# Performance work log

Hardware: AMD Instinct MI355X
Metric: run time of the kernel (lower is better)

Reference implementation:

```python
import jax, jax.numpy as jnp
import numpy as np

D = 1024
E = 8
K = 2
NUM_ITER = 2
DT = 0.1
H = 64           # controller_hidden
CTX = 2 * D


def _gelu(t):
    return jax.nn.gelu(t, approximate=False)


def _inl(ctrl, x, v, mu):
    # ctrl: [T, 3D] -> alpha, beta, gate chunks of size D
    alpha_raw, beta_raw, gate_raw = jnp.split(ctrl, 3, axis=-1)
    alpha = jax.nn.sigmoid(alpha_raw)
    beta = jax.nn.softplus(beta_raw)
    gate = jax.nn.sigmoid(gate_raw)
    error = x - mu
    v_next = alpha * v - beta * error
    x_next = x + DT * gate * v_next
    return x_next, v_next


def setup_inputs() -> dict:
    key = jax.random.key(0)
    ks = jax.random.split(key, 20)
    s = 0.02
    inp = {
        'x': jax.random.normal(ks[0], (4, 4096, D), jnp.float32),
        # router MLP
        'w_r1': jax.random.normal(ks[1], (D, D // 4), jnp.float32) * s,
        'b_r1': jnp.zeros((D // 4,), jnp.float32),
        'w_r2': jax.random.normal(ks[2], (D // 4, E), jnp.float32) * s,
        'b_r2': jnp.zeros((E,), jnp.float32),
        # halt gate MLP
        'w_h1': jax.random.normal(ks[3], (D, D // 4), jnp.float32) * s,
        'b_h1': jnp.zeros((D // 4,), jnp.float32),
        'w_h2': jax.random.normal(ks[4], (D // 4, 1), jnp.float32) * s,
        'b_h2': jnp.zeros((1,), jnp.float32),
        # expert tables
        'expert_w1': jax.random.normal(ks[5], (E, CTX, H), jnp.float32) * s,
        'expert_b1': jnp.zeros((E, H), jnp.float32),
        'expert_w2': jax.random.normal(ks[6], (E, H, 3 * D), jnp.float32) * s,
        'expert_b2': jnp.zeros((E, 3 * D), jnp.float32),
        # shared expert
        'w_s1': jax.random.normal(ks[7], (CTX, H), jnp.float32) * s,
        'b_s1': jnp.zeros((H,), jnp.float32),
        'w_s2': jax.random.normal(ks[8], (H, 3 * D), jnp.float32) * s,
        'b_s2': jnp.zeros((3 * D,), jnp.float32),
        'shared_weight': jnp.asarray(0.5, jnp.float32),
        # refine MLP
        'w_f1': jax.random.normal(ks[9], (D, 2 * D), jnp.float32) * s,
        'b_f1': jnp.zeros((2 * D,), jnp.float32),
        'w_f2': jax.random.normal(ks[10], (2 * D, D), jnp.float32) * s,
        'b_f2': jnp.zeros((D,), jnp.float32),
        'integration_weight': jnp.full((D,), 0.5, jnp.float32),
        'mu': jnp.zeros((D,), jnp.float32),
    }
    return inp


def reference(x, w_r1, b_r1, w_r2, b_r2, w_h1, b_h1, w_h2, b_h2,
              expert_w1, expert_b1, expert_w2, expert_b2,
              w_s1, b_s1, w_s2, b_s2, shared_weight,
              w_f1, b_f1, w_f2, b_f2, integration_weight, mu):
    B, N, Dm = x.shape
    xf = x.reshape(B * N, Dm)                       # [T, D]

    # router: top-k over softmax probs, renormalized
    logits = _gelu(xf @ w_r1 + b_r1) @ w_r2 + b_r2  # [T, E]
    probs = jax.nn.softmax(logits, axis=-1)
    top_p, top_i = jax.lax.top_k(probs, K)          # [T, K]
    top_p = top_p / jnp.sum(top_p, axis=-1, keepdims=True)

    flat_idx = top_i.reshape(-1)                    # [T*K]
    flat_w = top_p.reshape(-1, 1)                   # [T*K, 1]

    v = jnp.zeros_like(xf)
    integrated = xf
    for _ in range(NUM_ITER):
        ctx = jnp.concatenate([integrated, v], axis=-1)     # [T, 2D]

        # shared expert path
        shared_ctrl = _gelu(ctx @ w_s1 + b_s1) @ w_s2 + b_s2
        x_shared, v_shared = _inl(shared_ctrl, integrated, v, mu)
        sw = jax.nn.sigmoid(shared_weight)

        # routed experts: gather per-token weights, per-token matvec
        ctx_e = jnp.repeat(ctx, K, axis=0)                  # [T*K, 2D]
        x_e = jnp.repeat(integrated, K, axis=0)
        v_e = jnp.repeat(v, K, axis=0)
        w1 = expert_w1[flat_idx]                            # [T*K, 2D, H]
        b1 = expert_b1[flat_idx]
        w2 = expert_w2[flat_idx]                            # [T*K, H, 3D]
        b2 = expert_b2[flat_idx]
        hidden = _gelu(jnp.einsum('tc,tch->th', ctx_e, w1) + b1)
        ctrl = jnp.einsum('th,tho->to', hidden, w2) + b2    # [T*K, 3D]
        x_r, v_r = _inl(ctrl, x_e, v_e, mu)
        x_r = (x_r * flat_w).reshape(B * N, K, Dm).sum(axis=1)
        v_r = (v_r * flat_w).reshape(B * N, K, Dm).sum(axis=1)

        x_next = sw * x_shared + (1.0 - sw) * x_r
        v_next = sw * v_shared + (1.0 - sw) * v_r

        halt = jax.nn.sigmoid(_gelu(x_next @ w_h1 + b_h1) @ w_h2 + b_h2)  # [T,1]
        refined = _gelu(x_next @ w_f1 + b_f1) @ w_f2 + b_f2               # [T,D]
        integrated = integrated + halt * refined * integration_weight
        v = v_next

    return integrated.reshape(B, N, Dm)
```

## Files before the change

kernel.cpp:

```cpp
#include <hip/hip_runtime.h>


#define TOK   16384
#define DDIM  1024
#define NEXP  8
#define DTC   0.1f
#define NDESC 320
#define GPAD  20480

using f32x4 = __attribute__((ext_vector_type(4))) float;
using bfv8  = __attribute__((ext_vector_type(8))) short;

__device__ __forceinline__ unsigned short f2bf(float x){
  unsigned u = __builtin_bit_cast(unsigned, x);
  u += 0x7fffu + ((u >> 16) & 1u);
  return (unsigned short)(u >> 16);
}
__device__ __forceinline__ float bf2f(unsigned short h){
  return __builtin_bit_cast(float, ((unsigned)h) << 16);
}
__device__ __forceinline__ float sigmf(float x){ return 1.0f/(1.0f+__expf(-x)); }
__device__ __forceinline__ float geluf(float x){
  float u = 1.595769122f * __builtin_fmaf(0.044715f*x*x, x, x);
  return x * sigmf(u);
}
__device__ __forceinline__ float softpf(float x){
  return fmaxf(x, 0.0f) + __logf(1.0f + __expf(-fabsf(x)));
}
__device__ __forceinline__ f32x4 mfma16(bfv8 a, bfv8 b, f32x4 c){
  return __builtin_amdgcn_mfma_f32_16x16x32_bf16(a, b, c, 0, 0, 0);
}
typedef __attribute__((address_space(1))) const void gvoid_t;
typedef __attribute__((address_space(3))) void svoid_t;
__device__ __forceinline__ void gload16(const void* g, void* l){
  __builtin_amdgcn_global_load_lds((gvoid_t*)g, (svoid_t*)l, 16, 0, 0);
}

__global__ __launch_bounds__(256) void transpose_cast(
    const float* __restrict__ src, unsigned short* __restrict__ dst, int R, int C)
{
  __shared__ float tile[32][33];
  size_t bo = (size_t)blockIdx.z * R * C;
  const float* s = src + bo;
  unsigned short* d = dst + bo;
  int c0 = blockIdx.x * 32, r0 = blockIdx.y * 32;
  int tx = threadIdx.x, ty = threadIdx.y;
  #pragma unroll
  for (int j = 0; j < 4; j++)
    tile[ty + 8*j][tx] = s[(size_t)(r0 + ty + 8*j) * C + c0 + tx];
  __syncthreads();
  #pragma unroll
  for (int j = 0; j < 4; j++)
    d[(size_t)(c0 + ty + 8*j) * R + r0 + tx] = f2bf(tile[tx][ty + 8*j]);
}

__global__ __launch_bounds__(256) void xinit_k(
    const float* __restrict__ xf, unsigned short* __restrict__ xb)
{
  const int n = TOK * 256;
  for (int i = blockIdx.x * 256 + threadIdx.x; i < n; i += gridDim.x * 256) {
    float4 f = ((const float4*)xf)[i];
    ushort4 u = {f2bf(f.x), f2bf(f.y), f2bf(f.z), f2bf(f.w)};
    ((ushort4*)xb)[i] = u;
  }
}

__global__ __launch_bounds__(256) void ctxb_k(
    const float* __restrict__ xf, const int* __restrict__ tokmap,
    unsigned short* __restrict__ ctx)
{
  const int g = blockIdx.x, tid = threadIdx.x;
  const int t = tokmap[g];
  if (tid < 128) {
    uint4 o4 = {0,0,0,0};
    if (t >= 0) {
      const float4* s = (const float4*)(xf + (size_t)t * 1024) + tid * 2;
      float4 f0 = s[0], f1 = s[1];
      unsigned short tmp[8] = {f2bf(f0.x), f2bf(f0.y), f2bf(f0.z), f2bf(f0.w),
                               f2bf(f1.x), f2bf(f1.y), f2bf(f1.z), f2bf(f1.w)};
      o4 = *(uint4*)tmp;
    }
    *(uint4*)&ctx[(size_t)g * 2048 + tid * 8] = o4;
  } else {
    *(uint4*)&ctx[(size_t)g * 2048 + 1024 + (tid - 128) * 8] = uint4{0,0,0,0};
  }
}

template<int EPI>
__global__ __launch_bounds__(256) void gemm_k(
    const unsigned short* __restrict__ A, int lda,
    const unsigned short* __restrict__ BT,
    const float* __restrict__ bias, const float* __restrict__ bias2,
    int Kd, int N,
    unsigned short* __restrict__ obf, unsigned short* __restrict__ obf2,
    const float* __restrict__ halt, const float* __restrict__ iw,
    float* __restrict__ integ, unsigned short* __restrict__ ctxX,
    const int* __restrict__ pf)
{
  __shared__ unsigned short As[128][64];
  __shared__ unsigned short Bs[128][64];
  const int total = gridDim.x * gridDim.y;
  const int bid = blockIdx.y * gridDim.x + blockIdx.x;
  const int swz = (bid & 7) * (total >> 3) + (bid >> 3);
  const int bx = swz % gridDim.x, by = swz / gridDim.x;

  const int tid  = threadIdx.x, lane = tid & 63, w = tid >> 6;
  const int wm   = w >> 1, wn = w & 1;
  const int gm0  = by * 128, gn0 = bx * 128;
  const int r8   = lane >> 3;
  const int sseg = (lane & 7) ^ r8;

  const unsigned short* aga[4];
  const unsigned short* bga[4];
  #pragma unroll
  for (int c = 0; c < 4; c++) {
    aga[c] = A  + (size_t)(gm0 + w*32 + c*8 + r8) * lda + sseg*8;
    bga[c] = BT + (size_t)(gn0 + w*32 + c*8 + r8) * Kd  + sseg*8;
  }

  f32x4 acc[4][4];
  #pragma unroll
  for (int i = 0; i < 4; i++)
    #pragma unroll
    for (int j = 0; j < 4; j++)
      acc[i][j] = f32x4{0.f,0.f,0.f,0.f};

  const int xr = (lane & 7) << 3;
  for (int k0 = 0; k0 < Kd; k0 += 64) {
    #pragma unroll
    for (int c = 0; c < 4; c++) gload16(aga[c] + k0, &As[w*32 + c*8][0]);
    #pragma unroll
    for (int c = 0; c < 4; c++) gload16(bga[c] + k0, &Bs[w*32 + c*8][0]);
    __syncthreads();
    #pragma unroll
    for (int kk = 0; kk < 64; kk += 32) {
      const int kof = kk + ((lane >> 4) << 3);
      bfv8 a[4], b[4];
      #pragma unroll
      for (int mf = 0; mf < 4; mf++)
        a[mf] = *(const bfv8*)&As[wm*64 + mf*16 + (lane & 15)][kof ^ xr];
      #pragma unroll
      for (int nf = 0; nf < 4; nf++)
        b[nf] = *(const bfv8*)&Bs[wn*64 + nf*16 + (lane & 15)][kof ^ xr];
      #pragma unroll
      for (int mf = 0; mf < 4; mf++)
        #pragma unroll
        for (int nf = 0; nf < 4; nf++)
          acc[mf][nf] = mfma16(a[mf], b[nf], acc[mf][nf]);
    }
    __syncthreads();
  }

  #pragma unroll
  for (int mf = 0; mf < 4; mf++) {
    #pragma unroll
    for (int nf = 0; nf < 4; nf++) {
      int col = gn0 + wn*64 + nf*16 + (lane & 15);
      float bc;
      if (EPI == 2) bc = (col < 2048) ? bias[col] : bias2[col - 2048];
      else          bc = bias[col];
      #pragma unroll
      for (int r = 0; r < 4; r++) {
        int row = gm0 + wm*64 + mf*16 + ((lane >> 4) << 2) + r;
        float v = acc[mf][nf][r] + bc;
        if (EPI == 0) {
          obf[(size_t)row * N + col] = f2bf(geluf(v));
        } else if (EPI == 2) {
          if (col < 2048) obf [(size_t)row * 2048 + col]         = f2bf(geluf(v));
          else            obf2[(size_t)row * 256 + (col - 2048)] = f2bf(geluf(v));
        } else {
          size_t ix = (size_t)row * DDIM + col;
          float nv = integ[ix] + halt[row] * v * iw[col];
          integ[ix] = nv;
          if (ctxX) ctxX[(size_t)pf[row] * 2048 + col] = f2bf(nv);
        }
      }
    }
  }
}

__global__ __launch_bounds__(256) void router_k(
    const unsigned short* __restrict__ h1, const float* __restrict__ w_r2,
    const float* __restrict__ b_r2, int* __restrict__ topi, float* __restrict__ topw)
{
  int t = blockIdx.x * 4 + (threadIdx.x >> 6);
  int lane = threadIdx.x & 63;
  const unsigned short* hp = h1 + (size_t)t * 256 + lane * 4;
  float hv[4];
  #pragma unroll
  for (int j = 0; j < 4; j++) hv[j] = bf2f(hp[j]);
  float acc[8];
  #pragma unroll
  for (int e = 0; e < 8; e++) acc[e] = 0.f;
  #pragma unroll
  for (int j = 0; j < 4; j++) {
    const float* wr = w_r2 + (size_t)(lane*4 + j) * 8;
    #pragma unroll
    for (int e = 0; e < 8; e++) acc[e] += hv[j] * wr[e];
  }
  #pragma unroll
  for (int off = 32; off > 0; off >>= 1)
    #pragma unroll
    for (int e = 0; e < 8; e++) acc[e] += __shfl_xor(acc[e], off);
  if (lane == 0) {
    float lg[8];
    #pragma unroll
    for (int e = 0; e < 8; e++) lg[e] = acc[e] + b_r2[e];
    int i0 = 0; float m0 = lg[0];
    #pragma unroll
    for (int e = 1; e < 8; e++) if (lg[e] > m0) { m0 = lg[e]; i0 = e; }
    int i1 = -1; float m1 = -3.4e38f;
    #pragma unroll
    for (int e = 0; e < 8; e++) if (e != i0 && lg[e] > m1) { m1 = lg[e]; i1 = e; }
    float w0 = 1.0f / (1.0f + expf(m1 - m0));
    topi[t*2] = i0; topi[t*2+1] = i1;
    topw[t*2] = w0; topw[t*2+1] = 1.0f - w0;
  }
}

__global__ __launch_bounds__(256) void haltgate_k(
    const unsigned short* __restrict__ h1, const float* __restrict__ w_h2,
    const float* __restrict__ b_h2, float* __restrict__ halt)
{
  int t = blockIdx.x * 4 + (threadIdx.x >> 6);
  int lane = threadIdx.x & 63;
  const unsigned short* hp = h1 + (size_t)t * 256 + lane * 4;
  float s = 0.f;
  #pragma unroll
  for (int j = 0; j < 4; j++) s += bf2f(hp[j]) * w_h2[lane*4 + j];
  #pragma unroll
  for (int off = 32; off > 0; off >>= 1) s += __shfl_xor(s, off);
  if (lane == 0) halt[t] = sigmf(s + b_h2[0]);
}

__global__ __launch_bounds__(256) void pairb_k(
    const int* __restrict__ topi, const float* __restrict__ topw,
    int* __restrict__ cnt, int* __restrict__ plist, float* __restrict__ wA)
{
  int t = blockIdx.x * 256 + threadIdx.x;
  int a = topi[2*t], b = topi[2*t+1];
  float wa = topw[2*t];
  if (a > b) { int tmp = a; a = b; b = tmp; wa = 1.0f - wa; }
  int pid = a * 8 + b;
  int pos = atomicAdd(&cnt[pid], 1);
  plist[pid * TOK + pos] = t;
  wA[t] = wa;
}

__global__ void desc_k(const int* __restrict__ cnt, int4* __restrict__ desc,
                       int* __restrict__ ndesc, int* __restrict__ pbase)
{
  if (threadIdx.x == 0 && blockIdx.x == 0) {
    int nt = 0, rb = 0;
    for (int p = 0; p < 64; p++) {
      pbase[p] = rb;
      int c = cnt[p];
      for (int o = 0; o < c; o += 64) {
        int rem = c - o; if (rem > 64) rem = 64;
        desc[nt] = make_int4(p, rb + o, rem, 0);
        nt++;
      }
      rb += (c + 63) & ~63;
    }
    ndesc[0] = nt;
  }
}

__global__ __launch_bounds__(256) void pmap_k(
    const int* __restrict__ cnt, const int* __restrict__ pbase,
    const int* __restrict__ plist, int* __restrict__ tokmap, int* __restrict__ pf)
{
  int pid = blockIdx.x;
  int pos = blockIdx.y * 256 + threadIdx.x;
  if (pos < cnt[pid]) {
    int t = plist[pid * TOK + pos];
    int g = pbase[pid] + pos;
    tokmap[g] = t;
    pf[t] = g;
  }
}

__global__ __launch_bounds__(256) void exp1t_k(
    const unsigned short* __restrict__ ctx,
    const int4* __restrict__ desc, const int* __restrict__ ndesc,
    const unsigned short* __restrict__ ew1T, const float* __restrict__ eb1,
    const unsigned short* __restrict__ ws1T, const float* __restrict__ bs1,
    unsigned short* __restrict__ hiddenG)
{
  __shared__ unsigned short As[64][64];
  __shared__ unsigned short Bs[192][64];
  const int dx = blockIdx.x;
  if (dx >= ndesc[0]) return;
  int4 dd = desc[dx];
  const int pid = dd.x, rbt = dd.y;
  const int e0 = pid >> 3, e1 = pid & 7;
  const unsigned short* w1b[3] = { ew1T + (size_t)e0 * 64 * 2048,
                                   ew1T + (size_t)e1 * 64 * 2048, ws1T };
  const float* b1b[3] = { eb1 + e0 * 64, eb1 + e1 * 64, bs1 };
  const int tid = threadIdx.x, lane = tid & 63, w = tid >> 6;

  const int arow = w*8 + (lane >> 3);
  const int sseg = (lane & 7) ^ (lane >> 3);
  const unsigned short* asrc[2];
  #pragma unroll
  for (int q = 0; q < 2; q++)
    asrc[q] = ctx + (size_t)(rbt + q*32 + arow) * 2048 + sseg * 8;
  const unsigned short* bsrc[3][2];
  #pragma unroll
  for (int p = 0; p < 3; p++)
    #pragma unroll
    for (int q = 0; q < 2; q++)
      bsrc[p][q] = w1b[p] + (size_t)(q*32 + arow) * 2048 + sseg * 8;

  f32x4 acc[3][4];
  #pragma unroll
  for (int p = 0; p < 3; p++)
    #pragma unroll
    for (int j = 0; j < 4; j++)
      acc[p][j] = f32x4{0.f,0.f,0.f,0.f};

  const int xr = (lane & 7) << 3;
  for (int k0 = 0; k0 < 2048; k0 += 64) {
    #pragma unroll
    for (int q = 0; q < 2; q++) gload16(asrc[q] + k0, &As[q*32 + w*8][0]);
    #pragma unroll
    for (int p = 0; p < 3; p++)
      #pragma unroll
      for (int q = 0; q < 2; q++)
        gload16(bsrc[p][q] + k0, &Bs[p*64 + q*32 + w*8][0]);
    __syncthreads();
    #pragma unroll
    for (int kk = 0; kk < 64; kk += 32) {
      const int kof = kk + ((lane >> 4) << 3);
      bfv8 a = *(const bfv8*)&As[w*16 + (lane & 15)][kof ^ xr];
      #pragma unroll
      for (int p = 0; p < 3; p++)
        #pragma unroll
        for (int nf = 0; nf < 4; nf++) {
          bfv8 b = *(const bfv8*)&Bs[p*64 + nf*16 + (lane & 15)][kof ^ xr];
          acc[p][nf] = mfma16(a, b, acc[p][nf]);
        }
    }
    __syncthreads();
  }

  #pragma unroll
  for (int p = 0; p < 3; p++) {
    #pragma unroll
    for (int nf = 0; nf < 4; nf++) {
      int col = nf*16 + (lane & 15);
      float bb = b1b[p][col];
      #pragma unroll
      for (int r = 0; r < 4; r++) {
        int row = w*16 + ((lane >> 4) << 2) + r;
        hiddenG[(size_t)(3*rbt + p*64 + row) * 64 + col] =
            f2bf(geluf(acc[p][nf][r] + bb));
      }
    }
  }
}

__global__ __launch_bounds__(256) void exp2r_k(
    const unsigned short* __restrict__ hiddenG,
    const int4* __restrict__ desc, const int* __restrict__ ndesc,
    const int* __restrict__ tokmap, const float* __restrict__ wA,
    const unsigned short* __restrict__ ew2T, const float* __restrict__ eb2,
    const unsigned short* __restrict__ ws2T, const float* __restrict__ bs2,
    const float* __restrict__ swp, const float* __restrict__ mu,
    unsigned short* __restrict__ ctx, unsigned short* __restrict__ xaccB)
{
  __shared__ unsigned short W2s[3][192][64];
  __shared__ int   s_tok[64];
  __shared__ float s_w[64];
  const int zq = blockIdx.x, dx = blockIdx.y;
  if (dx >= ndesc[0]) return;
  int4 dd = desc[dx];
  const int pid = dd.x, rbt = dd.y, cnt = dd.z;
  const int e0 = pid >> 3, e1 = pid & 7;
  const int tid = threadIdx.x, lane = tid & 63, w = tid >> 6;
  const float sw = sigmf(swp[0]);

  if (tid < 64) {
    int t = tokmap[rbt + tid]; if (t < 0) t = 0;
    s_tok[tid] = t; s_w[tid] = wA[t];
  }

  const unsigned short* w2b[3] = { ew2T + (size_t)e0*3072*64,
                                   ew2T + (size_t)e1*3072*64, ws2T };
  const float* b2b[3] = { eb2 + e0*3072, eb2 + e1*3072, bs2 };
  const int d0q  = zq * 256;
  const int srow = w*8 + (lane >> 3);
  const int sseg = (lane & 7) ^ (lane >> 3);
  const int xr   = (lane & 7) << 3;
  const int cr4  = (lane >> 4) << 2;
  const int arow = w*16 + (lane & 15);
  const int kof8 = (lane >> 4) << 3;

  bfv8 afr[3][2];
  #pragma unroll
  for (int p = 0; p < 3; p++)
    #pragma unroll
    for (int kk = 0; kk < 2; kk++)
      afr[p][kk] = *(const bfv8*)&hiddenG[
          (size_t)(3*rbt + p*64 + arow) * 64 + kk*32 + kof8];

  auto STAGE = [&](int b, int dcq, int path) {
    const int d00 = d0q + dcq*64;
    const unsigned short* w2 = w2b[path];
    #pragma unroll
    for (int q = 0; q < 6; q++) {
      int row  = q*32 + srow;
      int grow = (row >> 6)*1024 + d00 + (row & 63);
      gload16(w2 + (size_t)grow*64 + sseg*8, &W2s[b][q*32 + w*8][0]);
    }
  };

  STAGE(0, 0, 0);
  STAGE(1, 0, 1);
  int toks[4]; float wa4[4];
  float xx[4][4], vv[4][4];

  #pragma unroll
  for (int dcq = 0; dcq < 4; dcq++) {
    const int d00 = d0q + dcq*64;
    f32x4 A4[4], B4[4], C4[4], D4[4];
    #pragma unroll
    for (int cf = 0; cf < 4; cf++) {
      A4[cf] = f32x4{0.f,0.f,0.f,0.f}; B4[cf] = f32x4{0.f,0.f,0.f,0.f};
      C4[cf] = f32x4{0.f,0.f,0.f,0.f}; D4[cf] = f32x4{0.f,0.f,0.f,0.f};
    }
    #pragma unroll
    for (int path = 0; path < 3; path++) {
      const int ph = dcq*3 + path;
      if (ph == 0) {
        __syncthreads();
      } else if (ph == 11) {
        asm volatile("s_waitcnt vmcnt(0)" ::: "memory");
        __builtin_amdgcn_s_barrier();
        __builtin_amdgcn_sched_barrier(0);
      } else {
        asm volatile("s_waitcnt vmcnt(6)" ::: "memory");
        __builtin_amdgcn_s_barrier();
        __builtin_amdgcn_sched_barrier(0);
      }
      if (ph == 0) {
        #pragma unroll
        for (int r = 0; r < 4; r++) {
          int row = w*16 + cr4 + r;
          toks[r] = s_tok[row]; wa4[r] = s_w[row];
        }
        #pragma unroll
        for (int cf = 0; cf < 4; cf++) {
          int d = d00 + cf*16 + (lane & 15);
          #pragma unroll
          for (int r = 0; r < 4; r++) {
            size_t g = (size_t)(rbt + w*16 + cr4 + r);
            xx[cf][r] = bf2f(ctx[g*2048 + d]);
            vv[cf][r] = bf2f(ctx[g*2048 + 1024 + d]);
          }
        }
      }
      if (ph < 10) {
        const int phn = ph + 2;
        STAGE(phn % 3, phn / 3, phn % 3);
      }
      f32x4 acc[12];
      #pragma unroll
      for (int j = 0; j < 12; j++) acc[j] = f32x4{0.f,0.f,0.f,0.f};
      #pragma unroll
      for (int kk = 0; kk < 2; kk++) {
        const int kof = kk*32 + kof8;
        #pragma unroll
        for (int nf = 0; nf < 12; nf++) {
          bfv8 b = *(const bfv8*)&W2s[ph % 3][nf*16 + (lane & 15)][kof ^ xr];
          acc[nf] = mfma16(afr[path][kk], b, acc[nf]);
        }
      }
      const float* b2 = b2b[path];
      #pragma unroll
      for (int cf = 0; cf < 4; cf++) {
        int d = d00 + cf*16 + (lane & 15);
        float ba = b2[d], bb = b2[1024 + d], bg = b2[2048 + d];
        #pragma unroll
        for (int r = 0; r < 4; r++) {
          float cw = (path == 0) ? (1.f - sw) * wa4[r]
                   : (path == 1) ? (1.f - sw) * (1.f - wa4[r]) : sw;
          float al = sigmf(acc[cf][r] + ba);
          float be = softpf(acc[4 + cf][r] + bb);
          float ga = sigmf(acc[8 + cf][r] + bg);
          A4[cf][r] += cw * al;       B4[cf][r] += cw * be;
          C4[cf][r] += cw * ga * al;  D4[cf][r] += cw * ga * be;
        }
      }
    }
    #pragma unroll
    for (int cf = 0; cf < 4; cf++) {
      int d = d00 + cf*16 + (lane & 15);
      float muv = mu[d];
      #pragma unroll
      for (int r = 0; r < 4; r++) {
        int row = w*16 + cr4 + r;
        size_t g = (size_t)(rbt + row);
        float err = xx[cf][r] - muv;
        float vt = vv[cf][r] * A4[cf][r] - err * B4[cf][r];
        float gv = vv[cf][r] * C4[cf][r] - err * D4[cf][r];
        if (row < cnt) {
          xaccB[(size_t)toks[r]*1024 + d] = f2bf(xx[cf][r] + DTC * gv);
          ctx[g*2048 + 1024 + d]          = f2bf(vt);
        }
      }
    }
    if (dcq < 3) {
      const int dn = d00 + 64;
      #pragma unroll
      for (int cf = 0; cf < 4; cf++) {
        int d = dn + cf*16 + (lane & 15);
        #pragma unroll
        for (int r = 0; r < 4; r++) {
          size_t g = (size_t)(rbt + w*16 + cr4 + r);
          xx[cf][r] = bf2f(ctx[g*2048 + d]);
          vv[cf][r] = bf2f(ctx[g*2048 + 1024 + d]);
        }
      }
    }
  }
}

extern "C" void kernel_launch(void* const* d_in, const int* in_sizes, int n_in,
                              void* d_out, int out_size, void* d_ws, size_t ws_size,
                              hipStream_t stream)
{
  const float* x    = (const float*)d_in[0];
  const float* w_r1 = (const float*)d_in[1];
  const float* b_r1 = (const float*)d_in[2];
  const float* w_r2 = (const float*)d_in[3];
  const float* b_r2 = (const float*)d_in[4];
  const float* w_h1 = (const float*)d_in[5];
  const float* b_h1 = (const float*)d_in[6];
  const float* w_h2 = (const float*)d_in[7];
  const float* b_h2 = (const float*)d_in[8];
  const float* ew1  = (const float*)d_in[9];
  const float* eb1  = (const float*)d_in[10];
  const float* ew2  = (const float*)d_in[11];
  const float* eb2  = (const float*)d_in[12];
  const float* w_s1 = (const float*)d_in[13];
  const float* b_s1 = (const float*)d_in[14];
  const float* w_s2 = (const float*)d_in[15];
  const float* b_s2 = (const float*)d_in[16];
  const float* swt  = (const float*)d_in[17];
  const float* w_f1 = (const float*)d_in[18];
  const float* b_f1 = (const float*)d_in[19];
  const float* w_f2 = (const float*)d_in[20];
  const float* b_f2 = (const float*)d_in[21];
  const float* iw   = (const float*)d_in[22];
  const float* mu   = (const float*)d_in[23];
  float* out = (float*)d_out;

  char* ws = (char*)d_ws;
  size_t off = 0;
  auto take = [&](size_t bytes) -> char* {
    char* p = ws + off;
    off = (off + bytes + 255) & ~(size_t)255;
    return p;
  };
  const size_t TD4 = (size_t)TOK * DDIM * 4;
  unsigned short* xaccB = (unsigned short*)take((size_t)TOK * 1024 * 2);
  unsigned short* ctx   = (unsigned short*)take((size_t)GPAD * 2048 * 2);
  unsigned short* rh    = (unsigned short*)take((size_t)TOK * 2048 * 2);
  unsigned short* hiddenG = (unsigned short*)take((size_t)3 * GPAD * 64 * 2);
  unsigned short* h1 = (unsigned short*)take((size_t)TOK * 256 * 2);
  float* halt = (float*)take((size_t)TOK * 4);
  int*   topi = (int*)take((size_t)TOK * 2 * 4);
  float* topw = (float*)take((size_t)TOK * 2 * 4);
  int*   cnt  = (int*)take(64 * 4);
  int*   ndsc = (int*)take(64);
  int*   pbase= (int*)take(64 * 4);
  int4*  desc = (int4*)take((size_t)NDESC * 16);
  int*   plist= (int*)take((size_t)64 * TOK * 4);
  float* wAa  = (float*)take((size_t)TOK * 4);
  int*   tokmap = (int*)take((size_t)GPAD * 4);
  int*   pf     = (int*)take((size_t)TOK * 4);
  unsigned short* w_r1T = (unsigned short*)take((size_t)256 * 1024 * 2);
  unsigned short* wFH   = (unsigned short*)take((size_t)2304 * 1024 * 2);
  unsigned short* w_f2T = (unsigned short*)take((size_t)1024 * 2048 * 2);
  unsigned short* w_s1T = (unsigned short*)take((size_t)64 * 2048 * 2);
  unsigned short* w_s2T = (unsigned short*)take((size_t)3072 * 64 * 2);
  unsigned short* ew1T  = (unsigned short*)take((size_t)NEXP * 64 * 2048 * 2);
  unsigned short* ew2T  = (unsigned short*)take((size_t)NEXP * 3072 * 64 * 2);
  if (off > ws_size) return;

  hipMemcpyAsync(out, x, TD4, hipMemcpyDeviceToDevice, stream);
  hipMemsetAsync(cnt, 0, 64 * 4, stream);
  hipMemsetAsync(tokmap, 0xFF, (size_t)GPAD * 4, stream);

  dim3 tb(32, 8);
  transpose_cast<<<dim3(  8, 32, 1), tb, 0, stream>>>(w_r1, w_r1T, 1024,  256);
  transpose_cast<<<dim3( 64, 32, 1), tb, 0, stream>>>(w_f1, wFH, 1024, 2048);
  transpose_cast<<<dim3(  8, 32, 1), tb, 0, stream>>>(w_h1, wFH + (size_t)2048*1024, 1024, 256);
  transpose_cast<<<dim3( 32, 64, 1), tb, 0, stream>>>(w_f2, w_f2T, 2048, 1024);
  transpose_cast<<<dim3(  2, 64, 1), tb, 0, stream>>>(w_s1, w_s1T, 2048,   64);
  transpose_cast<<<dim3( 96,  2, 1), tb, 0, stream>>>(w_s2, w_s2T,   64, 3072);
  transpose_cast<<<dim3(  2, 64, 8), tb, 0, stream>>>(ew1,  ew1T,  2048,   64);
  transpose_cast<<<dim3( 96,  2, 8), tb, 0, stream>>>(ew2,  ew2T,    64, 3072);

  xinit_k<<<2048, 256, 0, stream>>>(x, xaccB);
  gemm_k<0><<<dim3(2, 128), 256, 0, stream>>>(
      xaccB, 1024, w_r1T, b_r1, nullptr, 1024, 256, h1, nullptr,
      nullptr, nullptr, nullptr, nullptr, nullptr);
  router_k<<<TOK / 4, 256, 0, stream>>>(h1, w_r2, b_r2, topi, topw);
  pairb_k<<<TOK / 256, 256, 0, stream>>>(topi, topw, cnt, plist, wAa);
  desc_k<<<1, 64, 0, stream>>>(cnt, desc, ndsc, pbase);
  pmap_k<<<dim3(64, 64), 256, 0, stream>>>(cnt, pbase, plist, tokmap, pf);
  ctxb_k<<<GPAD, 256, 0, stream>>>(out, tokmap, ctx);

  for (int it = 0; it < 2; it++) {
    exp1t_k<<<NDESC, 256, 0, stream>>>(ctx, desc, ndsc,
                                       ew1T, eb1, w_s1T, b_s1, hiddenG);
    exp2r_k<<<dim3(4, NDESC), 256, 0, stream>>>(
        hiddenG, desc, ndsc, tokmap, wAa, ew2T, eb2, w_s2T, b_s2,
        swt, mu, ctx, xaccB);
    gemm_k<2><<<dim3(18, 128), 256, 0, stream>>>(
        xaccB, 1024, wFH, b_f1, b_h1, 1024, 2304, rh, h1,
        nullptr, nullptr, nullptr, nullptr, nullptr);
    haltgate_k<<<TOK / 4, 256, 0, stream>>>(h1, w_h2, b_h2, halt);
    gemm_k<1><<<dim3(8, 128), 256, 0, stream>>>(
        rh, 2048, w_f2T, b_f2, nullptr, 2048, 1024, nullptr, nullptr,
        halt, iw, out, (it == 0) ? ctx : nullptr, pf);
  }
}
```

Baseline: 1.276 ms.

## Split-K the expert first-layer GEMM and reduce partials in second-layer kernel

The first expert layer (K=2048) is split into four K-slices across a 2D grid, so four times as many blocks work on it. Each slice writes fp32 partial sums into a buffer that aliases the refine-hidden workspace. The second-layer kernel sums the four partials, adds the bias and applies GELU before the MFMA. This trades extra fp32 partial traffic and a reduction for more parallelism in a kernel that previously launched only about 320 blocks.

```diff
diff --git a/kernel.cpp b/kernel.cpp
--- a/kernel.cpp
+++ b/kernel.cpp
@@ -280,23 +280,22 @@
   }
 }
 
-__global__ __launch_bounds__(256) void exp1t_k(
+__global__ __launch_bounds__(256) void exp1s_k(
     const unsigned short* __restrict__ ctx,
     const int4* __restrict__ desc, const int* __restrict__ ndesc,
-    const unsigned short* __restrict__ ew1T, const float* __restrict__ eb1,
-    const unsigned short* __restrict__ ws1T, const float* __restrict__ bs1,
-    unsigned short* __restrict__ hiddenG)
+    const unsigned short* __restrict__ ew1T,
+    const unsigned short* __restrict__ ws1T,
+    float* __restrict__ part)
 {
   __shared__ unsigned short As[64][64];
   __shared__ unsigned short Bs[192][64];
-  const int dx = blockIdx.x;
+  const int ks = blockIdx.x, dx = blockIdx.y;
   if (dx >= ndesc[0]) return;
   int4 dd = desc[dx];
   const int pid = dd.x, rbt = dd.y;
   const int e0 = pid >> 3, e1 = pid & 7;
   const unsigned short* w1b[3] = { ew1T + (size_t)e0 * 64 * 2048,
                                    ew1T + (size_t)e1 * 64 * 2048, ws1T };
-  const float* b1b[3] = { eb1 + e0 * 64, eb1 + e1 * 64, bs1 };
   const int tid = threadIdx.x, lane = tid & 63, w = tid >> 6;
 
   const int arow = w*8 + (lane >> 3);
@@ -320,7 +319,8 @@
       acc[p][j] = f32x4{0.f,0.f,0.f,0.f};
 
   const int xr = (lane & 7) << 3;
-  for (int k0 = 0; k0 < 2048; k0 += 64) {
+  const int kbeg = ks * 512, kend = kbeg + 512;
+  for (int k0 = kbeg; k0 < kend; k0 += 64) {
     #pragma unroll
     for (int q = 0; q < 2; q++) gload16(asrc[q] + k0, &As[q*32 + w*8][0]);
     #pragma unroll
@@ -344,28 +344,28 @@
     __syncthreads();
   }
 
+  float* pb = part + (size_t)ks * (3*GPAD) * 64;
   #pragma unroll
   for (int p = 0; p < 3; p++) {
     #pragma unroll
     for (int nf = 0; nf < 4; nf++) {
       int col = nf*16 + (lane & 15);
-      float bb = b1b[p][col];
       #pragma unroll
       for (int r = 0; r < 4; r++) {
         int row = w*16 + ((lane >> 4) << 2) + r;
-        hiddenG[(size_t)(3*rbt + p*64 + row) * 64 + col] =
-            f2bf(geluf(acc[p][nf][r] + bb));
+        pb[(size_t)(3*rbt + p*64 + row) * 64 + col] = acc[p][nf][r];
       }
     }
   }
 }
 
 __global__ __launch_bounds__(256) void exp2r_k(
-    const unsigned short* __restrict__ hiddenG,
+    const float* __restrict__ part,
     const int4* __restrict__ desc, const int* __restrict__ ndesc,
     const int* __restrict__ tokmap, const float* __restrict__ wA,
     const unsigned short* __restrict__ ew2T, const float* __restrict__ eb2,
     const unsigned short* __restrict__ ws2T, const float* __restrict__ bs2,
+    const float* __restrict__ eb1, const float* __restrict__ bs1,
     const float* __restrict__ swp, const float* __restrict__ mu,
     unsigned short* __restrict__ ctx, unsigned short* __restrict__ xaccB)
 {
@@ -388,6 +388,7 @@
   const unsigned short* w2b[3] = { ew2T + (size_t)e0*3072*64,
                                    ew2T + (size_t)e1*3072*64, ws2T };
   const float* b2b[3] = { eb2 + e0*3072, eb2 + e1*3072, bs2 };
+  const float* b1b[3] = { eb1 + e0*64, eb1 + e1*64, bs1 };
   const int d0q  = zq * 256;
   const int srow = w*8 + (lane >> 3);
   const int sseg = (lane & 7) ^ (lane >> 3);
@@ -398,11 +399,28 @@
 
   bfv8 afr[3][2];
   #pragma unroll
-  for (int p = 0; p < 3; p++)
-    #pragma unroll
-    for (int kk = 0; kk < 2; kk++)
-      afr[p][kk] = *(const bfv8*)&hiddenG[
-          (size_t)(3*rbt + p*64 + arow) * 64 + kk*32 + kof8];
+  for (int p = 0; p < 3; p++) {
+    const size_t rowb = (size_t)(3*rbt + p*64 + arow) * 64;
+    #pragma unroll
+    for (int kk = 0; kk < 2; kk++) {
+      const int c0 = kk*32 + kof8;
+      float s[8];
+      #pragma unroll
+      for (int j = 0; j < 8; j++) s[j] = b1b[p][c0 + j];
+      #pragma unroll
+      for (int ks = 0; ks < 4; ks++) {
+        const float* pp = part + (size_t)ks*(3*GPAD)*64 + rowb + c0;
+        float4 q0 = *(const float4*)pp;
+        float4 q1 = *(const float4*)(pp + 4);
+        s[0]+=q0.x; s[1]+=q0.y; s[2]+=q0.z; s[3]+=q0.w;
+        s[4]+=q1.x; s[5]+=q1.y; s[6]+=q1.z; s[7]+=q1.w;
+      }
+      unsigned short t8[8];
+      #pragma unroll
+      for (int j = 0; j < 8; j++) t8[j] = f2bf(geluf(s[j]));
+      afr[p][kk] = *(const bfv8*)t8;
+    }
+  }
 
   auto STAGE = [&](int b, int dcq, int path) {
     const int d00 = d0q + dcq*64;
@@ -567,7 +585,7 @@
   unsigned short* xaccB = (unsigned short*)take((size_t)TOK * 1024 * 2);
   unsigned short* ctx   = (unsigned short*)take((size_t)GPAD * 2048 * 2);
   unsigned short* rh    = (unsigned short*)take((size_t)TOK * 2048 * 2);
-  unsigned short* hiddenG = (unsigned short*)take((size_t)3 * GPAD * 64 * 2);
+  float* part = (float*)rh;
   unsigned short* h1 = (unsigned short*)take((size_t)TOK * 256 * 2);
   float* halt = (float*)take((size_t)TOK * 4);
   int*   topi = (int*)take((size_t)TOK * 2 * 4);
@@ -614,11 +632,11 @@
   ctxb_k<<<GPAD, 256, 0, stream>>>(out, tokmap, ctx);
 
   for (int it = 0; it < 2; it++) {
-    exp1t_k<<<NDESC, 256, 0, stream>>>(ctx, desc, ndsc,
-                                       ew1T, eb1, w_s1T, b_s1, hiddenG);
+    exp1s_k<<<dim3(4, NDESC), 256, 0, stream>>>(
+        ctx, desc, ndsc, ew1T, w_s1T, part);
     exp2r_k<<<dim3(4, NDESC), 256, 0, stream>>>(
-        hiddenG, desc, ndsc, tokmap, wAa, ew2T, eb2, w_s2T, b_s2,
-        swt, mu, ctx, xaccB);
+        part, desc, ndsc, tokmap, wAa, ew2T, eb2, w_s2T, b_s2,
+        eb1, b_s1, swt, mu, ctx, xaccB);
     gemm_k<2><<<dim3(18, 128), 256, 0, stream>>>(
         xaccB, 1024, wFH, b_f1, b_h1, 1024, 2304, rh, h1,
         nullptr, nullptr, nullptr, nullptr, nullptr);
```

Result: slower. 1.305 ms (+2.3%).

## Cut register pressure in exp2r kernel by splitting accumulators and deferring loads

Applied to the files above, without the earlier changes.

Splits the 12-fragment MFMA accumulator array into two halves of 6 and processes the epilogue per half. Hidden A-fragments are now reloaded from global memory each phase instead of being held for all three paths. The x/v context prefetch registers and token indices are dropped; those values are loaded right before they are used in the output step. The aim is to lower VGPR usage for better occupancy or to avoid spills. The cost is extra global loads and less overlap of the ctx load latency with compute.

```diff
diff --git a/kernel.cpp b/kernel.cpp
--- a/kernel.cpp
+++ b/kernel.cpp
@@ -378,7 +378,8 @@
   const int pid = dd.x, rbt = dd.y, cnt = dd.z;
   const int e0 = pid >> 3, e1 = pid & 7;
   const int tid = threadIdx.x, lane = tid & 63, w = tid >> 6;
-  const float sw = sigmf(swp[0]);
+  const float sw  = sigmf(swp[0]);
+  const float swc = 1.0f - sw;
 
   if (tid < 64) {
     int t = tokmap[rbt + tid]; if (t < 0) t = 0;
@@ -396,14 +397,6 @@
   const int arow = w*16 + (lane & 15);
   const int kof8 = (lane >> 4) << 3;
 
-  bfv8 afr[3][2];
-  #pragma unroll
-  for (int p = 0; p < 3; p++)
-    #pragma unroll
-    for (int kk = 0; kk < 2; kk++)
-      afr[p][kk] = *(const bfv8*)&hiddenG[
-          (size_t)(3*rbt + p*64 + arow) * 64 + kk*32 + kof8];
-
   auto STAGE = [&](int b, int dcq, int path) {
     const int d00 = d0q + dcq*64;
     const unsigned short* w2 = w2b[path];
@@ -417,8 +410,7 @@
 
   STAGE(0, 0, 0);
   STAGE(1, 0, 1);
-  int toks[4]; float wa4[4];
-  float xx[4][4], vv[4][4];
+  float wa4[4];
 
   #pragma unroll
   for (int dcq = 0; dcq < 4; dcq++) {
@@ -445,51 +437,48 @@
       }
       if (ph == 0) {
         #pragma unroll
-        for (int r = 0; r < 4; r++) {
-          int row = w*16 + cr4 + r;
-          toks[r] = s_tok[row]; wa4[r] = s_w[row];
-        }
-        #pragma unroll
-        for (int cf = 0; cf < 4; cf++) {
-          int d = d00 + cf*16 + (lane & 15);
-          #pragma unroll
-          for (int r = 0; r < 4; r++) {
-            size_t g = (size_t)(rbt + w*16 + cr4 + r);
-            xx[cf][r] = bf2f(ctx[g*2048 + d]);
-            vv[cf][r] = bf2f(ctx[g*2048 + 1024 + d]);
-          }
-        }
+        for (int r = 0; r < 4; r++)
+          wa4[r] = s_w[w*16 + cr4 + r];
       }
       if (ph < 10) {
         const int phn = ph + 2;
         STAGE(phn % 3, phn / 3, phn % 3);
       }
-      f32x4 acc[12];
-      #pragma unroll
-      for (int j = 0; j < 12; j++) acc[j] = f32x4{0.f,0.f,0.f,0.f};
-      #pragma unroll
-      for (int kk = 0; kk < 2; kk++) {
-        const int kof = kk*32 + kof8;
+      bfv8 a0 = *(const bfv8*)&hiddenG[(size_t)(3*rbt + path*64 + arow)*64 + kof8];
+      bfv8 a1 = *(const bfv8*)&hiddenG[(size_t)(3*rbt + path*64 + arow)*64 + 32 + kof8];
+      const float* b2 = b2b[path];
+      #pragma unroll
+      for (int cfh = 0; cfh < 2; cfh++) {
+        f32x4 acc[6];
         #pragma unroll
-        for (int nf = 0; nf < 12; nf++) {
-          bfv8 b = *(const bfv8*)&W2s[ph % 3][nf*16 + (lane & 15)][kof ^ xr];
-          acc[nf] = mfma16(afr[path][kk], b, acc[nf]);
+        for (int j = 0; j < 6; j++) acc[j] = f32x4{0.f,0.f,0.f,0.f};
+        #pragma unroll
+        for (int kk = 0; kk < 2; kk++) {
+          const int kof = kk*32 + kof8;
+          #pragma unroll
+          for (int j = 0; j < 6; j++) {
+            int nf = cfh*2 + (j & 1) + (j >> 1) * 4;
+            bfv8 b = *(const bfv8*)&W2s[ph % 3][nf*16 + (lane & 15)][kof ^ xr];
+            acc[j] = mfma16(kk == 0 ? a0 : a1, b, acc[j]);
+          }
         }
-      }
-      const float* b2 = b2b[path];
-      #pragma unroll
-      for (int cf = 0; cf < 4; cf++) {
-        int d = d00 + cf*16 + (lane & 15);
-        float ba = b2[d], bb = b2[1024 + d], bg = b2[2048 + d];
         #pragma unroll
-        for (int r = 0; r < 4; r++) {
-          float cw = (path == 0) ? (1.f - sw) * wa4[r]
-                   : (path == 1) ? (1.f - sw) * (1.f - wa4[r]) : sw;
-          float al = sigmf(acc[cf][r] + ba);
-          float be = softpf(acc[4 + cf][r] + bb);
-          float ga = sigmf(acc[8 + cf][r] + bg);
-          A4[cf][r] += cw * al;       B4[cf][r] += cw * be;
-          C4[cf][r] += cw * ga * al;  D4[cf][r] += cw * ga * be;
+        for (int cj = 0; cj < 2; cj++) {
+          int cf = cfh*2 + cj;
+          int d = d00 + cf*16 + (lane & 15);
+          float ba = b2[d], bb = b2[1024 + d], bg = b2[2048 + d];
+          #pragma unroll
+          for (int r = 0; r < 4; r++) {
+            float cw = (path == 0) ? swc * wa4[r]
+                     : (path == 1) ? swc * (1.0f - wa4[r]) : sw;
+            float al = sigmf(acc[cj][r] + ba);
+            float be = softpf(acc[2 + cj][r] + bb);
+            float ga = sigmf(acc[4 + cj][r] + bg);
+            A4[cf][r] = __builtin_fmaf(cw, al, A4[cf][r]);
+            B4[cf][r] = __builtin_fmaf(cw, be, B4[cf][r]);
+            C4[cf][r] = __builtin_fmaf(cw * ga, al, C4[cf][r]);
+            D4[cf][r] = __builtin_fmaf(cw * ga, be, D4[cf][r]);
+          }
         }
       }
     }
@@ -501,25 +490,15 @@
       for (int r = 0; r < 4; r++) {
         int row = w*16 + cr4 + r;
         size_t g = (size_t)(rbt + row);
-        float err = xx[cf][r] - muv;
-        float vt = vv[cf][r] * A4[cf][r] - err * B4[cf][r];
-        float gv = vv[cf][r] * C4[cf][r] - err * D4[cf][r];
+        float xx = bf2f(ctx[g*2048 + d]);
+        float vv = bf2f(ctx[g*2048 + 1024 + d]);
+        float err = xx - muv;
+        float vt = vv * A4[cf][r] - err * B4[cf][r];
+        float gv = vv * C4[cf][r] - err * D4[cf][r];
         if (row < cnt) {
-          xaccB[(size_t)toks[r]*1024 + d] = f2bf(xx[cf][r] + DTC * gv);
-          ctx[g*2048 + 1024 + d]          = f2bf(vt);
-        }
-      }
-    }
-    if (dcq < 3) {
-      const int dn = d00 + 64;
-      #pragma unroll
-      for (int cf = 0; cf < 4; cf++) {
-        int d = dn + cf*16 + (lane & 15);
-        #pragma unroll
-        for (int r = 0; r < 4; r++) {
-          size_t g = (size_t)(rbt + w*16 + cr4 + r);
-          xx[cf][r] = bf2f(ctx[g*2048 + d]);
-          vv[cf][r] = bf2f(ctx[g*2048 + 1024 + d]);
+          int tok = s_tok[row];
+          xaccB[(size_t)tok*1024 + d] = f2bf(xx + DTC * gv);
+          ctx[g*2048 + 1024 + d]      = f2bf(vt);
         }
       }
     }
```

After: 1.297 ms. No clear change (+1.7%).
